# Performance work log

Measured on AMD Instinct MI355X. Metric: run time of the kernel, lower is better.

## Reference

```python
import jax, jax.numpy as jnp
import numpy as np

N_USERS = 100000
N_ITEMS = 50000
N_NODES = N_USERS + N_ITEMS
D = 64
N_LAYERS = 3
POP_BINS = 10
NNZ = 2000000
BATCH = 256
BIAS_SCALE = 1.0


def setup_inputs() -> dict:
    key = jax.random.key(0)
    ks = jax.random.split(key, 16)
    std = 0.01
    inp = {
        "user_emb": jax.random.normal(ks[0], (N_USERS, D), jnp.float32) * std,
        "item_emb": jax.random.normal(ks[1], (N_ITEMS, D), jnp.float32) * std,
        "user_bias": jnp.zeros((N_USERS, 1), jnp.float32),
        "item_bias": jnp.zeros((N_ITEMS, 1), jnp.float32),
        "pop_emb": jax.random.normal(ks[2], (POP_BINS, D), jnp.float32) * std,
        "uW1": jax.random.normal(ks[3], (D, D), jnp.float32) / np.sqrt(D),
        "ub1": jnp.zeros((D,), jnp.float32),
        "uW2": jax.random.normal(ks[4], (D, D), jnp.float32) / np.sqrt(D),
        "ub2": jnp.zeros((D,), jnp.float32),
        "iW1": jax.random.normal(ks[5], (D, D), jnp.float32) / np.sqrt(D),
        "ib1": jnp.zeros((D,), jnp.float32),
        "iW2": jax.random.normal(ks[6], (D, D), jnp.float32) / np.sqrt(D),
        "ib2": jnp.zeros((D,), jnp.float32),
        "gW1": jax.random.normal(ks[7], (2 * D, D), jnp.float32) / np.sqrt(2 * D),
        "gb1": jnp.zeros((D,), jnp.float32),
        "gW2": jax.random.normal(ks[8], (D, 1), jnp.float32) / np.sqrt(D),
        "gb2": jnp.zeros((1,), jnp.float32),
        "adj_vals": jax.random.uniform(ks[9], (NNZ,), jnp.float32),
        "adj_rows": jax.random.randint(ks[10], (NNZ,), 0, N_NODES, jnp.int32),
        "adj_cols": jax.random.randint(ks[11], (NNZ,), 0, N_NODES, jnp.int32),
        "item_pop_bins": jax.random.randint(ks[12], (N_ITEMS,), 0, POP_BINS, jnp.int32),
        "users": jax.random.randint(ks[13], (BATCH,), 0, N_USERS, jnp.int32),
    }
    return inp


def _spmm(vals, rows, cols, E):
    # sparse (N x N) @ E  via gather + segment-sum
    msgs = vals[:, None] * E[cols]          # [nnz, d]
    return jax.ops.segment_sum(msgs, rows, num_segments=N_NODES)


def _mlp2(x, W1, b1, W2, b2):
    return jax.nn.relu(x @ W1 + b1) @ W2 + b2


def reference(user_emb, item_emb, user_bias, item_bias, pop_emb,
              uW1, ub1, uW2, ub2, iW1, ib1, iW2, ib2,
              gW1, gb1, gW2, gb2,
              adj_vals, adj_rows, adj_cols, item_pop_bins, users):
    # ---- computer(): LightGCN propagation with uniform layer weights ----
    emb = jnp.concatenate([user_emb, item_emb], axis=0)   # [N, d]
    w = 1.0 / (N_LAYERS + 1)
    out = emb * w
    cur = emb
    for _ in range(N_LAYERS):
        cur = _spmm(adj_vals, adj_rows, adj_cols, cur)
        out = out + cur * w
    all_users, all_items = out[:N_USERS], out[N_USERS:]

    # ---- popularity-gated item fusion ----
    p_vec = pop_emb[item_pop_bins]                         # [n_items, d]
    gate_in = jnp.concatenate([all_items, p_vec], axis=-1)
    z = jax.nn.sigmoid(_mlp2(gate_in, gW1, gb1, gW2, gb2)) # [n_items, 1]
    items_fused = (1.0 - z) * all_items + z * p_vec

    # ---- two-tower scoring over all items ----
    U = _mlp2(all_users[users], uW1, ub1, uW2, ub2)        # [B, d]
    I = _mlp2(items_fused, iW1, ib1, iW2, ib2)             # [n_items, d]
    scores = U @ I.T                                        # [B, n_items]
    scores = scores + user_bias[users] * BIAS_SCALE + (item_bias.T) * BIAS_SCALE
    return scores
```

## Files before the change

### kernel.cpp

```cpp
#include <hip/hip_runtime.h>
#include <hip/hip_fp16.h>

#define N_USERS 100000
#define N_ITEMS 50000
#define N_NODES 150000
#define D 64
#define NNZ 2000000
#define BATCH 256
#define POP_BINS 10

#define BSH 9
#define NB2 293
#define CAP 8192
#define P1_EPB 4096
#define P1_BLOCKS 489

#define ST_P 130

__global__ __launch_bounds__(256) void k_p1(const int* __restrict__ rows,
                                            const int* __restrict__ cols,
                                            const float* __restrict__ vals,
                                            int* __restrict__ bcur,
                                            uint2* __restrict__ gstage) {
  __shared__ int cnt[NB2];
  __shared__ int gbase[NB2];
  int t = threadIdx.x;
  for (int i = t; i < NB2; i += 256) cnt[i] = 0;
  __syncthreads();
  int base = blockIdx.x * P1_EPB;
  for (int i = 0; i < 16; i++) {
    int e = base + i * 256 + t;
    if (e < NNZ) atomicAdd(&cnt[rows[e] >> BSH], 1);
  }
  __syncthreads();
  for (int i = t; i < NB2; i += 256) {
    int c = cnt[i];
    gbase[i] = c ? atomicAdd(&bcur[i], c) : 0;
    cnt[i] = 0;
  }
  __syncthreads();
  for (int i = 0; i < 16; i++) {
    int e = base + i * 256 + t;
    if (e < NNZ) {
      int r = rows[e];
      int b = r >> BSH;
      int rank = atomicAdd(&cnt[b], 1);
      unsigned key = ((unsigned)(r & 511) << 18) | (unsigned)cols[e];
      gstage[(size_t)b * CAP + gbase[b] + rank] =
          make_uint2(key, __float_as_uint(vals[e]));
    }
  }
}

__global__ __launch_bounds__(256) void k_p2(const int* __restrict__ bcur,
                                            const uint2* __restrict__ gstage,
                                            uint2* __restrict__ epack,
                                            int* __restrict__ rowbeg,
                                            int* __restrict__ rowend,
                                            int* __restrict__ gcursor,
                                            const int* __restrict__ users,
                                            int* __restrict__ uflag,
                                            int* __restrict__ ulist,
                                            int* __restrict__ ucnt) {
  int b = blockIdx.x, t = threadIdx.x;
  if (b == NB2) {
    int u = users[t];
    int old = atomicOr(&uflag[u >> 5], 1 << (u & 31));
    if (!((old >> (u & 31)) & 1)) {
      int p = atomicAdd(ucnt, 1);
      ulist[p] = u;
    }
    return;
  }
  __shared__ int cnt[512];
  __shared__ int off[512];
  __shared__ int s[256];
  __shared__ int gbs;
  __shared__ uint2 buf[CAP];
  int n = bcur[b];
  const uint2* gs = gstage + (size_t)b * CAP;
  if (t == 0) gbs = atomicAdd(gcursor, n);
  cnt[t] = 0;
  cnt[t + 256] = 0;
  __syncthreads();
  for (int j = t; j < n; j += 256)
    atomicAdd(&cnt[gs[j].x >> 18], 1);
  __syncthreads();
  int c0 = cnt[2 * t], c1 = cnt[2 * t + 1];
  s[t] = c0 + c1;
  __syncthreads();
  for (int o = 1; o < 256; o <<= 1) {
    int x = (t >= o) ? s[t - o] : 0;
    __syncthreads();
    s[t] += x;
    __syncthreads();
  }
  int ex = t ? s[t - 1] : 0;
  off[2 * t] = ex;
  off[2 * t + 1] = ex + c0;
  int base = gbs;
  int gr = (b << BSH) + 2 * t;
  if (gr < N_NODES) { rowbeg[gr] = base + ex; rowend[gr] = base + ex + c0; }
  if (gr + 1 < N_NODES) { rowbeg[gr + 1] = base + ex + c0; rowend[gr + 1] = base + ex + c0 + c1; }
  __syncthreads();
  for (int j = t; j < n; j += 256) {
    uint2 ed = gs[j];
    int lr = ed.x >> 18;
    int pos = atomicAdd(&off[lr], 1);
    buf[pos] = make_uint2(ed.x & 0x3FFFFu, ed.y);
  }
  __syncthreads();
  for (int j = t; j < n; j += 256) epack[base + j] = buf[j];
}

__global__ __launch_bounds__(256) void k_prep(const float* __restrict__ ue,
                                              const float* __restrict__ ie,
                                              __half* __restrict__ Eh,
                                              const float* __restrict__ pop,
                                              const float* __restrict__ gW1,
                                              const float* __restrict__ iW1,
                                              float* __restrict__ hp,
                                              float* __restrict__ pp1) {
  int b = blockIdx.x;
  if (b == 9375) {
    for (int idx = threadIdx.x; idx < 2 * POP_BINS * 64; idx += 256) {
      int q = idx;
      bool second = q >= POP_BINS * 64;
      if (second) q -= POP_BINS * 64;
      int bb = q >> 6, o = q & 63;
      float s = 0.f;
      if (!second) {
        for (int k = 0; k < 64; k++) s += pop[bb * 64 + k] * gW1[(64 + k) * 64 + o];
        hp[q] = s;
      } else {
        for (int k = 0; k < 64; k++) s += pop[bb * 64 + k] * iW1[k * 64 + o];
        pp1[q] = s;
      }
    }
    return;
  }
  int t = b * 256 + threadIdx.x;
  size_t fo = (size_t)t * 4;
  const float* src = (fo < (size_t)N_USERS * 64) ? ue + fo
                                                 : ie + (fo - (size_t)N_USERS * 64);
  float4 v = *(const float4*)src;
  __half2* dst = (__half2*)(Eh + fo);
  dst[0] = __floats2half2_rn(v.x, v.y);
  dst[1] = __floats2half2_rn(v.z, v.w);
}

#define SPMM_QW_BODY(TBL)                                                     \
  float a0 = 0.f, a1 = 0.f, a2 = 0.f, a3 = 0.f;                               \
  int j = beg;                                                                \
  for (; j + 7 < end; j += 8) {                                               \
    uint2 ea = epack[j + q];                                                  \
    uint2 eb = epack[j + 4 + q];                                              \
    uint2 ra = *(const uint2*)(TBL + (size_t)ea.x * 64 + 4 * p);              \
    uint2 rb = *(const uint2*)(TBL + (size_t)eb.x * 64 + 4 * p);              \
    float va = __uint_as_float(ea.y), vb = __uint_as_float(eb.y);             \
    float2 la = __half22float2(*(const __half2*)&ra.x);                       \
    float2 ha = __half22float2(*(const __half2*)&ra.y);                       \
    float2 lb = __half22float2(*(const __half2*)&rb.x);                       \
    float2 hb = __half22float2(*(const __half2*)&rb.y);                       \
    a0 += va * la.x; a1 += va * la.y; a2 += va * ha.x; a3 += va * ha.y;       \
    a0 += vb * lb.x; a1 += vb * lb.y; a2 += vb * hb.x; a3 += vb * hb.y;       \
  }                                                                           \
  for (; j < end; j += 4) {                                                   \
    int jj = j + q;                                                           \
    int jc = (jj < end) ? jj : end - 1;                                       \
    uint2 e = epack[jc];                                                      \
    float v = (jj < end) ? __uint_as_float(e.y) : 0.f;                        \
    uint2 r = *(const uint2*)(TBL + (size_t)e.x * 64 + 4 * p);                \
    float2 lo = __half22float2(*(const __half2*)&r.x);                        \
    float2 hi = __half22float2(*(const __half2*)&r.y);                        \
    a0 += v * lo.x; a1 += v * lo.y; a2 += v * hi.x; a3 += v * hi.y;           \
  }                                                                           \
  a0 += __shfl_xor(a0, 16, 64); a0 += __shfl_xor(a0, 32, 64);                 \
  a1 += __shfl_xor(a1, 16, 64); a1 += __shfl_xor(a1, 32, 64);                 \
  a2 += __shfl_xor(a2, 16, 64); a2 += __shfl_xor(a2, 32, 64);                 \
  a3 += __shfl_xor(a3, 16, 64); a3 += __shfl_xor(a3, 32, 64);

__global__ __launch_bounds__(256) void k_spmm1(const int* __restrict__ rowbeg,
                                               const int* __restrict__ rowend,
                                               const uint2* __restrict__ epack,
                                               const float* __restrict__ ue,
                                               const float* __restrict__ ie,
                                               const __half* __restrict__ Eh0,
                                               const int* __restrict__ uflag,
                                               __half* __restrict__ EoutH,
                                               float* __restrict__ Oacc) {
  int wave = blockIdx.x * 4 + (threadIdx.x >> 6);
  int row = __builtin_amdgcn_readfirstlane(wave);
  if (row >= N_NODES) return;
  int lane = threadIdx.x & 63;
  int p = lane & 15, q = lane >> 4;
  int beg = rowbeg[row];
  int end = rowend[row];
  SPMM_QW_BODY(Eh0)
  if (q == 0) {
    __half2* eo = (__half2*)(EoutH + (size_t)row * 64 + 4 * p);
    eo[0] = __floats2half2_rn(a0, a1);
    eo[1] = __floats2half2_rn(a2, a3);
    bool need = (row >= N_USERS) || (((uflag[row >> 5] >> (row & 31)) & 1) != 0);
    if (need) {
      const float* srow = (row < N_USERS) ? ue + (size_t)row * 64
                                          : ie + (size_t)(row - N_USERS) * 64;
      float4 sv = *(const float4*)(srow + 4 * p);
      *(float4*)(Oacc + (size_t)row * 64 + 4 * p) =
          make_float4(0.25f * (sv.x + a0), 0.25f * (sv.y + a1),
                      0.25f * (sv.z + a2), 0.25f * (sv.w + a3));
    }
  }
}

__global__ __launch_bounds__(256) void k_spmm2h(const int* __restrict__ rowbeg,
                                                const int* __restrict__ rowend,
                                                const uint2* __restrict__ epack,
                                                const __half* __restrict__ Ein,
                                                const int* __restrict__ uflag,
                                                __half* __restrict__ EoutH,
                                                float* __restrict__ Oacc) {
  int wave = blockIdx.x * 4 + (threadIdx.x >> 6);
  int row = __builtin_amdgcn_readfirstlane(wave);
  if (row >= N_NODES) return;
  int lane = threadIdx.x & 63;
  int p = lane & 15, q = lane >> 4;
  int beg = rowbeg[row];
  int end = rowend[row];
  SPMM_QW_BODY(Ein)
  if (q == 0) {
    __half2* eo = (__half2*)(EoutH + (size_t)row * 64 + 4 * p);
    eo[0] = __floats2half2_rn(a0, a1);
    eo[1] = __floats2half2_rn(a2, a3);
    if (row >= N_USERS || (((uflag[row >> 5] >> (row & 31)) & 1) != 0)) {
      float4* op = (float4*)(Oacc + (size_t)row * 64 + 4 * p);
      float4 cur = *op;
      *op = make_float4(cur.x + 0.25f * a0, cur.y + 0.25f * a1,
                        cur.z + 0.25f * a2, cur.w + 0.25f * a3);
    }
  }
}

__global__ __launch_bounds__(256) void k_spmm3h(const int* __restrict__ rowbeg,
                                                const int* __restrict__ rowend,
                                                const uint2* __restrict__ epack,
                                                const __half* __restrict__ Ein,
                                                const int* __restrict__ ulist,
                                                const int* __restrict__ ucnt,
                                                float* __restrict__ Oacc) {
  int w = blockIdx.x * 4 + (threadIdx.x >> 6);
  int row;
  if (w < N_ITEMS) {
    row = N_USERS + w;
  } else {
    int k = w - N_ITEMS;
    if (k >= ucnt[0]) return;
    row = ulist[k];
  }
  row = __builtin_amdgcn_readfirstlane(row);
  int lane = threadIdx.x & 63;
  int p = lane & 15, q = lane >> 4;
  int beg = rowbeg[row];
  int end = rowend[row];
  SPMM_QW_BODY(Ein)
  if (q == 0) {
    float4* op = (float4*)(Oacc + (size_t)row * 64 + 4 * p);
    float4 cur = *op;
    *op = make_float4(cur.x + 0.25f * a0, cur.y + 0.25f * a1,
                      cur.z + 0.25f * a2, cur.w + 0.25f * a3);
  }
}

__global__ __launch_bounds__(256) void k_user(const float* __restrict__ Oacc,
                                              const int* __restrict__ users,
                                              const float* __restrict__ ubias,
                                              const float* __restrict__ uW1,
                                              const float* __restrict__ ub1,
                                              const float* __restrict__ uW2,
                                              const float* __restrict__ ub2,
                                              float* __restrict__ Ut) {
  int ub = blockIdx.x * 4 + (threadIdx.x >> 6);
  int lane = threadIdx.x & 63;
  int u = users[ub];
  float x = Oacc[(size_t)u * 64 + lane];
  float h = ub1[lane];
#pragma unroll
  for (int k = 0; k < 64; k++)
    h = fmaf(__shfl(x, k, 64), uW1[k * 64 + lane], h);
  h = h > 0.f ? h : 0.f;
  float o = ub2[lane];
#pragma unroll
  for (int k = 0; k < 64; k++)
    o = fmaf(__shfl(h, k, 64), uW2[k * 64 + lane], o);
  Ut[lane * 256 + ub] = o;
  if (lane == 0) Ut[64 * 256 + ub] = ubias[u];
}

__global__ __launch_bounds__(256) void k_gemm12(const float* __restrict__ Oacc,
                                                const float* __restrict__ gW1,
                                                const float* __restrict__ iW1,
                                                const int* __restrict__ bins,
                                                const float* __restrict__ hp,
                                                const float* __restrict__ pp1,
                                                const float* __restrict__ gb1,
                                                const float* __restrict__ gW2,
                                                const float* __restrict__ gb2,
                                                const float* __restrict__ ib1,
                                                const float* __restrict__ iW2,
                                                const float* __restrict__ ib2,
                                                float* __restrict__ I) {
  __shared__ float Is[64 * ST_P];
  __shared__ float Bs[64 * 128];
  __shared__ float zp[128][9];
  __shared__ float zs[128];
  int tid = threadIdx.x;
  int i0 = blockIdx.x * 128;
  {
    int c4 = tid & 15, r0 = tid >> 4;
#pragma unroll
    for (int s = 0; s < 8; s++) {
      int r = r0 + s * 16;
      int it = i0 + r;
      float4 v = make_float4(0.f, 0.f, 0.f, 0.f);
      if (it < N_ITEMS) v = *(const float4*)(Oacc + (size_t)(N_USERS + it) * 64 + c4 * 4);
      Is[(c4 * 4 + 0) * ST_P + r] = v.x;
      Is[(c4 * 4 + 1) * ST_P + r] = v.y;
      Is[(c4 * 4 + 2) * ST_P + r] = v.z;
      Is[(c4 * 4 + 3) * ST_P + r] = v.w;
    }
  }
  for (int idx = tid; idx < 64 * 128; idx += 256) {
    int k = idx >> 7, o = idx & 127;
    Bs[idx] = (o < 64) ? gW1[k * 64 + o] : iW1[k * 64 + (o - 64)];
  }
  __syncthreads();
  int tx = tid & 15, ty = tid >> 4;
  float acc[8][8];
#pragma unroll
  for (int a = 0; a < 8; a++)
#pragma unroll
    for (int b = 0; b < 8; b++) acc[a][b] = 0.f;
  {
    const float* ip = Is + tx * 8;
    const float* wp = Bs + ty * 8;
#pragma unroll 2
    for (int k = 0; k < 64; k++) {
      float4 iv0 = *(const float4*)(ip + k * ST_P);
      float4 iv1 = *(const float4*)(ip + k * ST_P + 4);
      float4 wv0 = *(const float4*)(wp + k * 128);
      float4 wv1 = *(const float4*)(wp + k * 128 + 4);
      float iv[8] = {iv0.x, iv0.y, iv0.z, iv0.w, iv1.x, iv1.y, iv1.z, iv1.w};
      float wv[8] = {wv0.x, wv0.y, wv0.z, wv0.w, wv1.x, wv1.y, wv1.z, wv1.w};
#pragma unroll
      for (int a = 0; a < 8; a++)
#pragma unroll
        for (int b = 0; b < 8; b++) acc[a][b] += iv[a] * wv[b];
    }
  }
  int ibase = i0 + tx * 8;
  if (ty < 8) {
    int o0 = ty * 8;
#pragma unroll
    for (int a = 0; a < 8; a++) {
      int it = ibase + a;
      float p = 0.f;
      if (it < N_ITEMS) {
        int bin = bins[it];
        const float* hpr = hp + bin * 64 + o0;
#pragma unroll
        for (int b = 0; b < 8; b++) {
          float g = acc[a][b] + hpr[b] + gb1[o0 + b];
          g = g > 0.f ? g : 0.f;
          p += g * gW2[o0 + b];
        }
      }
      zp[tx * 8 + a][ty] = p;
    }
  }
  __syncthreads();
  if (tid < 128) {
    float s = gb2[0];
#pragma unroll
    for (int k = 0; k < 8; k++) s += zp[tid][k];
    zs[tid] = 1.f / (1.f + expf(-s));
  }
  __syncthreads();
  if (ty >= 8) {
    int o0 = (ty - 8) * 8;
#pragma unroll
    for (int a = 0; a < 8; a++) {
      int it = ibase + a;
      int item = tx * 8 + a;
      float z = zs[item];
      int bin = (it < N_ITEMS) ? bins[it] : 0;
      const float* ppr = pp1 + bin * 64 + o0;
#pragma unroll
      for (int b = 0; b < 8; b++) {
        float v = (1.f - z) * acc[a][b] + z * ppr[b] + ib1[o0 + b];
        Is[(o0 + b) * ST_P + item] = v > 0.f ? v : 0.f;
      }
    }
  }
  for (int idx = tid; idx < 64 * 64; idx += 256) Bs[idx] = iW2[idx];
  __syncthreads();
  float acc2[8][4];
#pragma unroll
  for (int a = 0; a < 8; a++)
#pragma unroll
    for (int b = 0; b < 4; b++) acc2[a][b] = 0.f;
  {
    const float* ip = Is + tx * 8;
    const float* wp = Bs + ty * 4;
#pragma unroll 2
    for (int k = 0; k < 64; k++) {
      float4 iv0 = *(const float4*)(ip + k * ST_P);
      float4 iv1 = *(const float4*)(ip + k * ST_P + 4);
      float4 wv = *(const float4*)(wp + k * 64);
      float iv[8] = {iv0.x, iv0.y, iv0.z, iv0.w, iv1.x, iv1.y, iv1.z, iv1.w};
      float wvv[4] = {wv.x, wv.y, wv.z, wv.w};
#pragma unroll
      for (int a = 0; a < 8; a++)
#pragma unroll
        for (int b = 0; b < 4; b++) acc2[a][b] += iv[a] * wvv[b];
    }
  }
  int oc = ty * 4;
  float b0 = ib2[oc], b1 = ib2[oc + 1], b2 = ib2[oc + 2], b3 = ib2[oc + 3];
#pragma unroll
  for (int a = 0; a < 8; a++) {
    int it = ibase + a;
    if (it < N_ITEMS) {
      float4 s0 = make_float4(acc2[a][0] + b0, acc2[a][1] + b1,
                              acc2[a][2] + b2, acc2[a][3] + b3);
      *(float4*)(I + (size_t)it * 64 + oc) = s0;
    }
  }
}

__global__ __launch_bounds__(256) void k_scores(const float* __restrict__ I,
                                                const float* __restrict__ Ut,
                                                const float* __restrict__ item_bias,
                                                float* __restrict__ out) {
  __shared__ float Is[64 * ST_P];
  __shared__ float Us[64 * 128];
  int tid = threadIdx.x;
  int i0 = blockIdx.x * 128;
  {
    int c4 = tid & 15, r0 = tid >> 4;
#pragma unroll
    for (int s = 0; s < 8; s++) {
      int r = r0 + s * 16;
      int it = i0 + r;
      float4 v = make_float4(0.f, 0.f, 0.f, 0.f);
      if (it < N_ITEMS) v = *(const float4*)(I + (size_t)it * 64 + c4 * 4);
      Is[(c4 * 4 + 0) * ST_P + r] = v.x;
      Is[(c4 * 4 + 1) * ST_P + r] = v.y;
      Is[(c4 * 4 + 2) * ST_P + r] = v.z;
      Is[(c4 * 4 + 3) * ST_P + r] = v.w;
    }
  }
  int tx = tid & 15;
  int ty = tid >> 4;
  int ibase = i0 + tx * 8;
  float ib[8];
#pragma unroll
  for (int a = 0; a < 8; a++)
    ib[a] = (ibase + a < N_ITEMS) ? item_bias[ibase + a] : 0.f;
  for (int uh = 0; uh < 2; uh++) {
    int ubase = uh * 128;
    if (uh) __syncthreads();
    {
      int u4 = tid & 31, k0 = tid >> 5;
#pragma unroll
      for (int s = 0; s < 8; s++) {
        int k = k0 + s * 8;
        float4 v = *(const float4*)(Ut + k * 256 + ubase + u4 * 4);
        *(float4*)(Us + k * 128 + u4 * 4) = v;
      }
    }
    __syncthreads();
    float acc[8][8];
#pragma unroll
    for (int a = 0; a < 8; a++)
#pragma unroll
      for (int b = 0; b < 8; b++) acc[a][b] = 0.f;
    const float* ip = Is + tx * 8;
    const float* up = Us + ty * 8;
#pragma unroll 2
    for (int k = 0; k < 64; k++) {
      float4 iv0 = *(const float4*)(ip + k * ST_P);
      float4 iv1 = *(const float4*)(ip + k * ST_P + 4);
      float4 uv0 = *(const float4*)(up + k * 128);
      float4 uv1 = *(const float4*)(up + k * 128 + 4);
      float iv[8] = {iv0.x, iv0.y, iv0.z, iv0.w, iv1.x, iv1.y, iv1.z, iv1.w};
      float uv[8] = {uv0.x, uv0.y, uv0.z, uv0.w, uv1.x, uv1.y, uv1.z, uv1.w};
#pragma unroll
      for (int a = 0; a < 8; a++)
#pragma unroll
        for (int b = 0; b < 8; b++) acc[a][b] += iv[a] * uv[b];
    }
#pragma unroll
    for (int bb = 0; bb < 8; bb++) {
      int bu = ubase + ty * 8 + bb;
      float ubias = Ut[64 * 256 + bu];
      float* orow = out + (size_t)bu * N_ITEMS + ibase;
      if (ibase + 7 < N_ITEMS) {
        float4 s0 = make_float4(acc[0][bb] + ubias + ib[0], acc[1][bb] + ubias + ib[1],
                                acc[2][bb] + ubias + ib[2], acc[3][bb] + ubias + ib[3]);
        float4 s1 = make_float4(acc[4][bb] + ubias + ib[4], acc[5][bb] + ubias + ib[5],
                                acc[6][bb] + ubias + ib[6], acc[7][bb] + ubias + ib[7]);
        *(float4*)orow = s0;
        *(float4*)(orow + 4) = s1;
      } else {
#pragma unroll
        for (int a = 0; a < 8; a++)
          if (ibase + a < N_ITEMS) orow[a] = acc[a][bb] + ubias + ib[a];
      }
    }
  }
}

extern "C" void kernel_launch(void* const* d_in, const int* in_sizes, int n_in,
                              void* d_out, int out_size, void* d_ws, size_t ws_size,
                              hipStream_t stream) {
  const float* user_emb  = (const float*)d_in[0];
  const float* item_emb  = (const float*)d_in[1];
  const float* user_bias = (const float*)d_in[2];
  const float* item_bias = (const float*)d_in[3];
  const float* pop_emb   = (const float*)d_in[4];
  const float* uW1 = (const float*)d_in[5];
  const float* ub1 = (const float*)d_in[6];
  const float* uW2 = (const float*)d_in[7];
  const float* ub2 = (const float*)d_in[8];
  const float* iW1 = (const float*)d_in[9];
  const float* ib1 = (const float*)d_in[10];
  const float* iW2 = (const float*)d_in[11];
  const float* ib2 = (const float*)d_in[12];
  const float* gW1 = (const float*)d_in[13];
  const float* gb1 = (const float*)d_in[14];
  const float* gW2 = (const float*)d_in[15];
  const float* gb2 = (const float*)d_in[16];
  const float* adj_vals = (const float*)d_in[17];
  const int* adj_rows = (const int*)d_in[18];
  const int* adj_cols = (const int*)d_in[19];
  const int* bins  = (const int*)d_in[20];
  const int* users = (const int*)d_in[21];
  float* out = (float*)d_out;

  float* ws = (float*)d_ws;
  float* Oacc = ws;
  float* bufA = ws + 9600000;
  float* bufB = ws + 19200000;
  uint2* epack = (uint2*)(ws + 28800000);
  int* rowbeg = (int*)(ws + 32800000);
  int* rowend = (int*)(ws + 32950000);
  int* uflag   = (int*)(ws + 33100000);
  int* ucnt    = (int*)(ws + 33103125);
  int* bcur    = (int*)(ws + 33103126);
  int* gcursor = (int*)(ws + 33103419);
  int* ulist   = (int*)(ws + 33103420);
  float* Ut   = ws + 33104000;
  float* hp   = ws + 33121000;
  float* pp1  = ws + 33122000;
  uint2* gstage = (uint2*)bufB;
  __half* Eh0 = (__half*)bufA;
  __half* E1h = (__half*)(bufA + 4800000);
  __half* E2h = (__half*)bufB;
  float* I  = bufB;

  hipMemsetAsync(uflag, 0, 3680 * sizeof(int), stream);
  k_prep<<<9376, 256, 0, stream>>>(user_emb, item_emb, Eh0, pop_emb, gW1, iW1, hp, pp1);
  k_p1<<<P1_BLOCKS, 256, 0, stream>>>(adj_rows, adj_cols, adj_vals, bcur, gstage);
  k_p2<<<NB2 + 1, 256, 0, stream>>>(bcur, gstage, epack, rowbeg, rowend, gcursor,
                                    users, uflag, ulist, ucnt);

  k_spmm1<<<37500, 256, 0, stream>>>(rowbeg, rowend, epack, user_emb, item_emb,
                                     Eh0, uflag, E1h, Oacc);
  k_spmm2h<<<37500, 256, 0, stream>>>(rowbeg, rowend, epack, E1h, uflag, E2h, Oacc);
  k_spmm3h<<<12564, 256, 0, stream>>>(rowbeg, rowend, epack, E2h, ulist, ucnt, Oacc);

  k_user<<<64, 256, 0, stream>>>(Oacc, users, user_bias, uW1, ub1, uW2, ub2, Ut);
  k_gemm12<<<391, 256, 0, stream>>>(Oacc, gW1, iW1, bins, hp, pp1, gb1, gW2, gb2,
                                    ib1, iW2, ib2, I);
  k_scores<<<391, 256, 0, stream>>>(I, Ut, item_bias, out);
}
```

Before: 476.4 us.

## Merge prep with bucketing pass, fold user MLP into item GEMM, shrink score tiles

Merges the fp16 conversion and pop-precompute kernel with the edge-bucketing pass into one launch, and folds the user-tower MLP into the item gemm kernel as extra blocks. This removes two kernel launches and lets independent work run concurrently. The scores kernel now uses 64-item tiles with 8x4 per-thread accumulators and 782 blocks instead of 391, to raise occupancy and parallelism, at the cost of reloading the user tile more times overall.

```diff
diff --git a/kernel.cpp b/kernel.cpp
--- a/kernel.cpp
+++ b/kernel.cpp
@@ -16,18 +16,56 @@
 #define P1_BLOCKS 489
 
 #define ST_P 130
-
-__global__ __launch_bounds__(256) void k_p1(const int* __restrict__ rows,
-                                            const int* __restrict__ cols,
-                                            const float* __restrict__ vals,
-                                            int* __restrict__ bcur,
-                                            uint2* __restrict__ gstage) {
+#define ST_P2 66
+
+__global__ __launch_bounds__(256) void k_prep_p1(const float* __restrict__ ue,
+                                                 const float* __restrict__ ie,
+                                                 __half* __restrict__ Eh,
+                                                 const float* __restrict__ pop,
+                                                 const float* __restrict__ gW1,
+                                                 const float* __restrict__ iW1,
+                                                 float* __restrict__ hp,
+                                                 float* __restrict__ pp1,
+                                                 const int* __restrict__ rows,
+                                                 const int* __restrict__ cols,
+                                                 const float* __restrict__ vals,
+                                                 int* __restrict__ bcur,
+                                                 uint2* __restrict__ gstage) {
   __shared__ int cnt[NB2];
   __shared__ int gbase[NB2];
+  int b = blockIdx.x;
   int t = threadIdx.x;
+  if (b < 9375) {
+    int idx = b * 256 + t;
+    size_t fo = (size_t)idx * 4;
+    const float* src = (fo < (size_t)N_USERS * 64) ? ue + fo
+                                                   : ie + (fo - (size_t)N_USERS * 64);
+    float4 v = *(const float4*)src;
+    __half2* dst = (__half2*)(Eh + fo);
+    dst[0] = __floats2half2_rn(v.x, v.y);
+    dst[1] = __floats2half2_rn(v.z, v.w);
+    return;
+  }
+  if (b == 9375) {
+    for (int idx = t; idx < 2 * POP_BINS * 64; idx += 256) {
+      int q = idx;
+      bool second = q >= POP_BINS * 64;
+      if (second) q -= POP_BINS * 64;
+      int bb = q >> 6, o = q & 63;
+      float s = 0.f;
+      if (!second) {
+        for (int k = 0; k < 64; k++) s += pop[bb * 64 + k] * gW1[(64 + k) * 64 + o];
+        hp[q] = s;
+      } else {
+        for (int k = 0; k < 64; k++) s += pop[bb * 64 + k] * iW1[k * 64 + o];
+        pp1[q] = s;
+      }
+    }
+    return;
+  }
+  int base = (b - 9376) * P1_EPB;
   for (int i = t; i < NB2; i += 256) cnt[i] = 0;
   __syncthreads();
-  int base = blockIdx.x * P1_EPB;
   for (int i = 0; i < 16; i++) {
     int e = base + i * 256 + t;
     if (e < NNZ) atomicAdd(&cnt[rows[e] >> BSH], 1);
@@ -43,10 +81,10 @@
     int e = base + i * 256 + t;
     if (e < NNZ) {
       int r = rows[e];
-      int b = r >> BSH;
-      int rank = atomicAdd(&cnt[b], 1);
+      int bb = r >> BSH;
+      int rank = atomicAdd(&cnt[bb], 1);
       unsigned key = ((unsigned)(r & 511) << 18) | (unsigned)cols[e];
-      gstage[(size_t)b * CAP + gbase[b] + rank] =
+      gstage[(size_t)bb * CAP + gbase[bb] + rank] =
           make_uint2(key, __float_as_uint(vals[e]));
     }
   }
@@ -111,42 +149,6 @@
   }
   __syncthreads();
   for (int j = t; j < n; j += 256) epack[base + j] = buf[j];
-}
-
-__global__ __launch_bounds__(256) void k_prep(const float* __restrict__ ue,
-                                              const float* __restrict__ ie,
-                                              __half* __restrict__ Eh,
-                                              const float* __restrict__ pop,
-                                              const float* __restrict__ gW1,
-                                              const float* __restrict__ iW1,
-                                              float* __restrict__ hp,
-                                              float* __restrict__ pp1) {
-  int b = blockIdx.x;
-  if (b == 9375) {
-    for (int idx = threadIdx.x; idx < 2 * POP_BINS * 64; idx += 256) {
-      int q = idx;
-      bool second = q >= POP_BINS * 64;
-      if (second) q -= POP_BINS * 64;
-      int bb = q >> 6, o = q & 63;
-      float s = 0.f;
-      if (!second) {
-        for (int k = 0; k < 64; k++) s += pop[bb * 64 + k] * gW1[(64 + k) * 64 + o];
-        hp[q] = s;
-      } else {
-        for (int k = 0; k < 64; k++) s += pop[bb * 64 + k] * iW1[k * 64 + o];
-        pp1[q] = s;
-      }
-    }
-    return;
-  }
-  int t = b * 256 + threadIdx.x;
-  size_t fo = (size_t)t * 4;
-  const float* src = (fo < (size_t)N_USERS * 64) ? ue + fo
-                                                 : ie + (fo - (size_t)N_USERS * 64);
-  float4 v = *(const float4*)src;
-  __half2* dst = (__half2*)(Eh + fo);
-  dst[0] = __floats2half2_rn(v.x, v.y);
-  dst[1] = __floats2half2_rn(v.z, v.w);
 }
 
 #define SPMM_QW_BODY(TBL)                                                     \
@@ -271,49 +273,49 @@
   }
 }
 
-__global__ __launch_bounds__(256) void k_user(const float* __restrict__ Oacc,
-                                              const int* __restrict__ users,
-                                              const float* __restrict__ ubias,
-                                              const float* __restrict__ uW1,
-                                              const float* __restrict__ ub1,
-                                              const float* __restrict__ uW2,
-                                              const float* __restrict__ ub2,
-                                              float* __restrict__ Ut) {
-  int ub = blockIdx.x * 4 + (threadIdx.x >> 6);
-  int lane = threadIdx.x & 63;
-  int u = users[ub];
-  float x = Oacc[(size_t)u * 64 + lane];
-  float h = ub1[lane];
-#pragma unroll
-  for (int k = 0; k < 64; k++)
-    h = fmaf(__shfl(x, k, 64), uW1[k * 64 + lane], h);
-  h = h > 0.f ? h : 0.f;
-  float o = ub2[lane];
-#pragma unroll
-  for (int k = 0; k < 64; k++)
-    o = fmaf(__shfl(h, k, 64), uW2[k * 64 + lane], o);
-  Ut[lane * 256 + ub] = o;
-  if (lane == 0) Ut[64 * 256 + ub] = ubias[u];
-}
-
-__global__ __launch_bounds__(256) void k_gemm12(const float* __restrict__ Oacc,
-                                                const float* __restrict__ gW1,
-                                                const float* __restrict__ iW1,
-                                                const int* __restrict__ bins,
-                                                const float* __restrict__ hp,
-                                                const float* __restrict__ pp1,
-                                                const float* __restrict__ gb1,
-                                                const float* __restrict__ gW2,
-                                                const float* __restrict__ gb2,
-                                                const float* __restrict__ ib1,
-                                                const float* __restrict__ iW2,
-                                                const float* __restrict__ ib2,
-                                                float* __restrict__ I) {
+__global__ __launch_bounds__(256) void k_gemm12u(const float* __restrict__ Oacc,
+                                                 const float* __restrict__ gW1,
+                                                 const float* __restrict__ iW1,
+                                                 const int* __restrict__ bins,
+                                                 const float* __restrict__ hp,
+                                                 const float* __restrict__ pp1,
+                                                 const float* __restrict__ gb1,
+                                                 const float* __restrict__ gW2,
+                                                 const float* __restrict__ gb2,
+                                                 const float* __restrict__ ib1,
+                                                 const float* __restrict__ iW2,
+                                                 const float* __restrict__ ib2,
+                                                 float* __restrict__ I,
+                                                 const int* __restrict__ users,
+                                                 const float* __restrict__ ubias,
+                                                 const float* __restrict__ uW1,
+                                                 const float* __restrict__ ub1,
+                                                 const float* __restrict__ uW2,
+                                                 const float* __restrict__ ub2,
+                                                 float* __restrict__ Ut) {
   __shared__ float Is[64 * ST_P];
   __shared__ float Bs[64 * 128];
   __shared__ float zp[128][9];
   __shared__ float zs[128];
   int tid = threadIdx.x;
+  if (blockIdx.x >= 391) {
+    int ub = (blockIdx.x - 391) * 4 + (tid >> 6);
+    int lane = tid & 63;
+    int u = users[ub];
+    float x = Oacc[(size_t)u * 64 + lane];
+    float h = ub1[lane];
+#pragma unroll
+    for (int k = 0; k < 64; k++)
+      h = fmaf(__shfl(x, k, 64), uW1[k * 64 + lane], h);
+    h = h > 0.f ? h : 0.f;
+    float o = ub2[lane];
+#pragma unroll
+    for (int k = 0; k < 64; k++)
+      o = fmaf(__shfl(h, k, 64), uW2[k * 64 + lane], o);
+    Ut[lane * 256 + ub] = o;
+    if (lane == 0) Ut[64 * 256 + ub] = ubias[u];
+    return;
+  }
   int i0 = blockIdx.x * 128;
   {
     int c4 = tid & 15, r0 = tid >> 4;
@@ -441,26 +443,26 @@
                                                 const float* __restrict__ Ut,
                                                 const float* __restrict__ item_bias,
                                                 float* __restrict__ out) {
-  __shared__ float Is[64 * ST_P];
+  __shared__ float Is[64 * ST_P2];
   __shared__ float Us[64 * 128];
   int tid = threadIdx.x;
-  int i0 = blockIdx.x * 128;
+  int i0 = blockIdx.x * 64;
   {
     int c4 = tid & 15, r0 = tid >> 4;
 #pragma unroll
-    for (int s = 0; s < 8; s++) {
+    for (int s = 0; s < 4; s++) {
       int r = r0 + s * 16;
       int it = i0 + r;
       float4 v = make_float4(0.f, 0.f, 0.f, 0.f);
       if (it < N_ITEMS) v = *(const float4*)(I + (size_t)it * 64 + c4 * 4);
-      Is[(c4 * 4 + 0) * ST_P + r] = v.x;
-      Is[(c4 * 4 + 1) * ST_P + r] = v.y;
-      Is[(c4 * 4 + 2) * ST_P + r] = v.z;
-      Is[(c4 * 4 + 3) * ST_P + r] = v.w;
-    }
-  }
-  int tx = tid & 15;
-  int ty = tid >> 4;
+      Is[(c4 * 4 + 0) * ST_P2 + r] = v.x;
+      Is[(c4 * 4 + 1) * ST_P2 + r] = v.y;
+      Is[(c4 * 4 + 2) * ST_P2 + r] = v.z;
+      Is[(c4 * 4 + 3) * ST_P2 + r] = v.w;
+    }
+  }
+  int tx = tid & 7;
+  int ty = tid >> 3;
   int ibase = i0 + tx * 8;
   float ib[8];
 #pragma unroll
@@ -479,29 +481,28 @@
       }
     }
     __syncthreads();
-    float acc[8][8];
+    float acc[8][4];
 #pragma unroll
     for (int a = 0; a < 8; a++)
 #pragma unroll
-      for (int b = 0; b < 8; b++) acc[a][b] = 0.f;
+      for (int b = 0; b < 4; b++) acc[a][b] = 0.f;
     const float* ip = Is + tx * 8;
-    const float* up = Us + ty * 8;
+    const float* up = Us + ty * 4;
 #pragma unroll 2
     for (int k = 0; k < 64; k++) {
-      float4 iv0 = *(const float4*)(ip + k * ST_P);
-      float4 iv1 = *(const float4*)(ip + k * ST_P + 4);
-      float4 uv0 = *(const float4*)(up + k * 128);
-      float4 uv1 = *(const float4*)(up + k * 128 + 4);
+      float4 iv0 = *(const float4*)(ip + k * ST_P2);
+      float4 iv1 = *(const float4*)(ip + k * ST_P2 + 4);
+      float4 uv = *(const float4*)(up + k * 128);
       float iv[8] = {iv0.x, iv0.y, iv0.z, iv0.w, iv1.x, iv1.y, iv1.z, iv1.w};
-      float uv[8] = {uv0.x, uv0.y, uv0.z, uv0.w, uv1.x, uv1.y, uv1.z, uv1.w};
+      float uvv[4] = {uv.x, uv.y, uv.z, uv.w};
 #pragma unroll
       for (int a = 0; a < 8; a++)
 #pragma unroll
-        for (int b = 0; b < 8; b++) acc[a][b] += iv[a] * uv[b];
-    }
-#pragma unroll
-    for (int bb = 0; bb < 8; bb++) {
-      int bu = ubase + ty * 8 + bb;
+        for (int b = 0; b < 4; b++) acc[a][b] += iv[a] * uvv[b];
+    }
+#pragma unroll
+    for (int bb = 0; bb < 4; bb++) {
+      int bu = ubase + ty * 4 + bb;
       float ubias = Ut[64 * 256 + bu];
       float* orow = out + (size_t)bu * N_ITEMS + ibase;
       if (ibase + 7 < N_ITEMS) {
@@ -569,8 +570,9 @@
   float* I  = bufB;
 
   hipMemsetAsync(uflag, 0, 3680 * sizeof(int), stream);
-  k_prep<<<9376, 256, 0, stream>>>(user_emb, item_emb, Eh0, pop_emb, gW1, iW1, hp, pp1);
-  k_p1<<<P1_BLOCKS, 256, 0, stream>>>(adj_rows, adj_cols, adj_vals, bcur, gstage);
+  k_prep_p1<<<9865, 256, 0, stream>>>(user_emb, item_emb, Eh0, pop_emb, gW1, iW1,
+                                      hp, pp1, adj_rows, adj_cols, adj_vals,
+                                      bcur, gstage);
   k_p2<<<NB2 + 1, 256, 0, stream>>>(bcur, gstage, epack, rowbeg, rowend, gcursor,
                                     users, uflag, ulist, ucnt);
 
@@ -579,8 +581,8 @@
   k_spmm2h<<<37500, 256, 0, stream>>>(rowbeg, rowend, epack, E1h, uflag, E2h, Oacc);
   k_spmm3h<<<12564, 256, 0, stream>>>(rowbeg, rowend, epack, E2h, ulist, ucnt, Oacc);
 
-  k_user<<<64, 256, 0, stream>>>(Oacc, users, user_bias, uW1, ub1, uW2, ub2, Ut);
-  k_gemm12<<<391, 256, 0, stream>>>(Oacc, gW1, iW1, bins, hp, pp1, gb1, gW2, gb2,
-                                    ib1, iW2, ib2, I);
-  k_scores<<<391, 256, 0, stream>>>(I, Ut, item_bias, out);
-}
+  k_gemm12u<<<455, 256, 0, stream>>>(Oacc, gW1, iW1, bins, hp, pp1, gb1, gW2, gb2,
+                                     ib1, iW2, ib2, I,
+                                     users, user_bias, uW1, ub1, uW2, ub2, Ut);
+  k_scores<<<782, 256, 0, stream>>>(I, Ut, item_bias, out);
+}
```

Result: slower. 517.8 us (+8.7%).
